# Optimization experiments

Measured on AMD Instinct MI355X. Metric: run time of the kernel, lower is better.

The kernel has to match this reference:

```python
import jax, jax.numpy as jnp
import numpy as np

A = 3                      # anchors per location
HS = [256, 128, 64, 32]    # square feature-map sizes (FPN levels)
B = 4                      # batch (num images)
SIZES = [A * h * h for h in HS]
T = sum(SIZES)             # 261120 anchors per image
PRE_N, POST_N = 512, 512
NMS_TH, SCORE_TH, MIN_SIZE = 0.7, 0.0, 1e-3
LOG_MAX = 4.135166556742356   # log(1000/16), standard delta clamp
MAXV = 8                      # max vertices of quad-quad intersection
LVL_OFF = 8192.0              # per-level coordinate offset for batched NMS


def box_corners(b):
    # b: [..., 5] (cx, cy, w, h, angle) -> [..., 4, 2] CCW corners
    cx, cy, w, h, a = (b[..., i] for i in range(5))
    c, s = jnp.cos(a), jnp.sin(a)
    dx = 0.5 * jnp.stack([w, -w, -w, w], -1)
    dy = 0.5 * jnp.stack([h, h, -h, -h], -1)
    x = cx[..., None] + dx * c[..., None] - dy * s[..., None]
    y = cy[..., None] + dx * s[..., None] + dy * c[..., None]
    return jnp.stack([x, y], -1)


def _clip(poly, cnt, p1, p2):
    # Sutherland-Hodgman clip of poly (padded [MAXV,2], cnt valid) by half-plane left of p1->p2
    e = p2 - p1
    d = e[0] * (poly[:, 1] - p1[1]) - e[1] * (poly[:, 0] - p1[0])
    def body(carry, i):
        out, oc = carry
        nxt = jnp.where(i + 1 < cnt, i + 1, 0)
        cur_in, nxt_in = d[i] >= 0, d[nxt] >= 0
        valid = i < cnt
        keep = valid & cur_in
        out = out.at[oc].set(jnp.where(keep, poly[i], out[oc]))
        oc = oc + keep.astype(jnp.int32)
        crs = valid & (cur_in != nxt_in)
        den = d[i] - d[nxt]
        t = d[i] / jnp.where(den == 0, 1.0, den)
        ip = poly[i] + t * (poly[nxt] - poly[i])
        out = out.at[oc].set(jnp.where(crs, ip, out[oc]))
        oc = oc + crs.astype(jnp.int32)
        return (out, oc), None
    (out, oc), _ = jax.lax.scan(body, (jnp.zeros((MAXV, 2), poly.dtype), jnp.int32(0)), jnp.arange(MAXV))
    return out, oc


def _inter_area(ca, cb):
    # intersection area of two convex quads given CCW corners [4,2]
    poly = jnp.zeros((MAXV, 2), ca.dtype).at[:4].set(ca)
    cnt = jnp.int32(4)
    for k in range(4):
        poly, cnt = _clip(poly, cnt, cb[k], cb[(k + 1) % 4])
    i = jnp.arange(MAXV)
    nxt = jnp.where(i + 1 < cnt, i + 1, 0)
    cr = poly[i, 0] * poly[nxt, 1] - poly[nxt, 0] * poly[i, 1]
    area = 0.5 * jnp.abs(jnp.sum(jnp.where(i < cnt, cr, 0.0)))
    return jnp.where(cnt >= 3, area, 0.0)


def decode(deltas, anchors):
    # XYWHA decode with 6-dim deltas (dx,dy,dw,dh,dsin,dcos), weights all 1.0
    ax, ay, aw, ah, aa = (anchors[..., i] for i in range(5))
    dx, dy, dw, dh, ds, dc = (deltas[..., i] for i in range(6))
    dw = jnp.minimum(dw, LOG_MAX)
    dh = jnp.minimum(dh, LOG_MAX)
    return jnp.stack([ax + dx * aw, ay + dy * ah, aw * jnp.exp(dw),
                      ah * jnp.exp(dh), aa + jnp.arctan2(ds, dc)], -1)


def nms_image(boxes, scores, levels):
    # boxes [N,5], scores [N] (post-sigmoid), levels [N] int32 -> fixed-size padded outputs
    N = scores.shape[0]
    valid = (boxes[:, 2] >= MIN_SIZE) & (boxes[:, 3] >= MIN_SIZE) & (scores >= SCORE_TH)
    s = jnp.where(valid, scores, -jnp.inf)
    order = jnp.argsort(-s)
    bx, sc, vd = boxes[order], s[order], valid[order]
    off = levels[order].astype(bx.dtype) * LVL_OFF
    nb = bx.at[:, :2].add(off[:, None])          # level offset => cross-level IoU == 0
    nbg = jax.lax.stop_gradient(nb)
    corners = box_corners(nbg)                    # [N,4,2]
    areas = nbg[:, 2] * nbg[:, 3]
    CH = 128
    def chunk_fn(args):
        cc, ca = args
        def row(ci, ai):
            inter = jax.vmap(lambda cj: _inter_area(ci, cj))(corners)
            return inter / (ai + areas - inter + 1e-7)
        return jax.vmap(row)(cc, ca)
    iou = jax.lax.map(chunk_fn, (corners.reshape(N // CH, CH, 4, 2),
                                 areas.reshape(N // CH, CH))).reshape(N, N)
    idx = jnp.arange(N)
    def body(i, sup):
        keep_i = ~sup[i]
        return sup | (keep_i & (iou[i] > NMS_TH) & (idx > i))
    sup = jax.lax.fori_loop(0, N, body, ~vd)      # invalid boxes start suppressed
    kept = ~sup
    _, top_i = jax.lax.top_k(jnp.where(kept, sc, -jnp.inf), POST_N)
    ok = kept[top_i]
    return jnp.where(ok[:, None], bx[top_i], 0.0), jnp.where(ok, sc[top_i], 0.0)


def rpn_forward(objs, dlts, anchors):
    obj_f, dlt_f = [], []
    for o, d, h in zip(objs, dlts, HS):
        # permute_and_flatten: [B,A,H,W] -> [B,H*W*A]; [B,A*6,H,W] -> [B,H*W*A,6]
        obj_f.append(o.transpose(0, 2, 3, 1).reshape(B, -1))
        dlt_f.append(d.reshape(B, A, 6, h, h).transpose(0, 3, 4, 1, 2).reshape(B, -1, 6))
    objectness = jnp.concatenate(obj_f, 1)        # [B, T]
    deltas = jnp.concatenate(dlt_f, 1)            # [B, T, 6]
    proposals = decode(deltas, anchors)           # [B, T, 5]
    parts, offset = [], 0
    for sz in SIZES:                               # per-level top-k
        k = min(PRE_N, sz)
        _, ti = jax.lax.top_k(objectness[:, offset:offset + sz], k)
        parts.append(ti + offset)
        offset += sz
    top_idx = jnp.concatenate(parts, 1)           # [B, 4*PRE_N]
    levels = jnp.concatenate([jnp.full((sz,), i, jnp.int32) for i, sz in enumerate(SIZES)])
    obj_top = jnp.take_along_axis(objectness, top_idx, 1)
    prop_top = jnp.take_along_axis(proposals, top_idx[..., None], 1)
    lvl_top = levels[top_idx]
    scores = jax.nn.sigmoid(obj_top)
    return jax.vmap(nms_image)(prop_top, scores, lvl_top)


def setup_inputs() -> dict:
    key = jax.random.key(0)
    ks = jax.random.split(key, 9)
    inp = {}
    for i, h in enumerate(HS):
        inp[f"obj{i}"] = jax.random.normal(ks[i], (B, A, h, h), jnp.float32)
        inp[f"dlt{i}"] = 0.25 * jax.random.normal(ks[4 + i], (B, A * 6, h, h), jnp.float32)
    u = jax.random.uniform(ks[8], (B, T, 5), jnp.float32)
    inp["anchors"] = jnp.stack([u[..., 0] * 1024.0, u[..., 1] * 1024.0,
                                8.0 + 120.0 * u[..., 2], 8.0 + 120.0 * u[..., 3],
                                jnp.pi * (u[..., 4] - 0.5)], -1)
    return inp


def reference(obj0, obj1, obj2, obj3, dlt0, dlt1, dlt2, dlt3, anchors):
    # returns (boxes [B, POST_N, 5], scores [B, POST_N]) padded with zeros
    return rpn_forward([obj0, obj1, obj2, obj3], [dlt0, dlt1, dlt2, dlt3], anchors)
```

## Files before the change

### kernel.cpp

```cpp
#include <hip/hip_runtime.h>

typedef unsigned int u32;
typedef unsigned long long u64;
typedef unsigned char u8;

#define NB 4
#define T_ANCH 261120
#define NCAND 2048
#define KSEL 512
#define POSTN 512
#define LOG_MAXF 4.135166556742356f
#define NMS_TH 0.7f
#define LVL_OFF_F 8192.0f
#define BINS 4096
#define EQCAP 8192
#define K5_BLOCKS 2048
#define K1_BLOCKS 256

__device__ __forceinline__ u32 mono32(float f){
  u32 u = __float_as_uint(f);
  return (u & 0x80000000u) ? ~u : (u | 0x80000000u);
}
__device__ __forceinline__ int lvl_hw(int lvl){ return 65536 >> (2*lvl); }
__device__ __forceinline__ int lvl_off(int lvl){
  return (lvl>0?196608:0) + (lvl>1?49152:0) + (lvl>2?12288:0);
}
__device__ __forceinline__ void k1_map(int bx, int& b, int& lvl, int& ch){
  b = bx >> 6;
  int c = bx & 63;
  if (c < 48){ lvl = 0; ch = c; }
  else if (c < 60){ lvl = 1; ch = c - 48; }
  else if (c < 63){ lvl = 2; ch = c - 60; }
  else { lvl = 3; ch = 0; }
}

__global__ __launch_bounds__(1024) void k1_hist_thresh(
    const float* __restrict__ o0, const float* __restrict__ o1,
    const float* __restrict__ o2, const float* __restrict__ o3,
    u32* __restrict__ hist16, u32* __restrict__ done16,
    u32* __restrict__ gb0, u32* __restrict__ gcA)
{
  int b, lvl, ch;
  k1_map(blockIdx.x, b, lvl, ch);
  int bid16 = b*4 + lvl;
  int nch = (lvl==0?48 : lvl==1?12 : lvl==2?3 : 1);
  const float* ob = (lvl==0)?o0 : (lvl==1)?o1 : (lvl==2)?o2 : o3;
  int hw = lvl_hw(lvl);
  int size = 3*hw;
  int n4 = size >> 2;
  int i4 = ch*1024 + threadIdx.x;
  __shared__ u32 hist[BINS];
  __shared__ u32 coarse[64];
  __shared__ int s_last;
  for (int i = threadIdx.x; i < BINS; i += 1024) hist[i] = 0;
  __syncthreads();
  if (i4 < n4){
    float4 v = ((const float4*)(ob + (size_t)b*size))[i4];
    atomicAdd(&hist[mono32(v.x) >> 20], 1u);
    atomicAdd(&hist[mono32(v.y) >> 20], 1u);
    atomicAdd(&hist[mono32(v.z) >> 20], 1u);
    atomicAdd(&hist[mono32(v.w) >> 20], 1u);
  }
  __syncthreads();
  u32* gh = hist16 + (size_t)bid16*BINS;
  for (int i = threadIdx.x; i < BINS; i += 1024){
    u32 c = hist[i];
    if (c) atomicAdd(&gh[i], c);
  }
  __syncthreads();
  if (threadIdx.x == 0){
    __threadfence();
    u32 d = atomicAdd(&done16[bid16], 1u);
    s_last = (d == (u32)(nch - 1)) ? 1 : 0;
  }
  __syncthreads();
  if (!s_last) return;

  __threadfence();
  for (int i = threadIdx.x; i < BINS; i += 1024)
    hist[i] = __hip_atomic_load(&gh[i], __ATOMIC_RELAXED, __HIP_MEMORY_SCOPE_AGENT);
  __syncthreads();
  int t = threadIdx.x;
  if (t < 64){
    u32 s = 0;
    for (int z = 0; z < 64; ++z) s += hist[t*64 + z];
    coarse[t] = s;
  }
  __syncthreads();
  if (t == 0){
    u32 acc = 0;
    int cb = 63;
    while (acc + coarse[cb] < (u32)KSEL){ acc += coarse[cb]; --cb; }
    int z = cb*64 + 63;
    while (acc + hist[z] < (u32)KSEL){ acc += hist[z]; --z; }
    gb0[bid16] = (u32)z;
    gcA[bid16] = acc;
  }
}

__global__ __launch_bounds__(1024) void k2_classify(
    const float* __restrict__ o0, const float* __restrict__ o1,
    const float* __restrict__ o2, const float* __restrict__ o3,
    const u32* __restrict__ gb0,
    u32* __restrict__ emitcnt, u32* __restrict__ tiecnt,
    int* __restrict__ cand_j, u64* __restrict__ gtie)
{
  int b, lvl, ch;
  k1_map(blockIdx.x, b, lvl, ch);
  int bid16 = b*4 + lvl;
  const float* ob = (lvl==0)?o0 : (lvl==1)?o1 : (lvl==2)?o2 : o3;
  int hw = lvl_hw(lvl);
  int size = 3*hw;
  int n4 = size >> 2;
  int i4 = ch*1024 + threadIdx.x;

  __shared__ u32 dbuf[KSEL];
  __shared__ u64 tbuf[4096];
  __shared__ u32 dn, tn, dbase, tbase;
  if (threadIdx.x == 0){ dn = 0; tn = 0; }
  __syncthreads();

  u32 b0v = gb0[bid16];
  if (i4 < n4){
    float4 v = ((const float4*)(ob + (size_t)b*size))[i4];
    int L = i4 << 2;
    int a = L / hw;
    int pix = L - a*hw;
    int j0 = pix*3 + a;
    float vv[4] = {v.x, v.y, v.z, v.w};
    #pragma unroll
    for (int q = 0; q < 4; ++q){
      u32 m = mono32(vv[q]);
      u32 bin = m >> 20;
      int j = j0 + 3*q;
      if (bin > b0v){
        u32 s = atomicAdd(&dn, 1u);
        if (s < (u32)KSEL) dbuf[s] = (u32)j;
      } else if (bin == b0v){
        u32 s = atomicAdd(&tn, 1u);
        if (s < 4096u) tbuf[s] = ((u64)m << 32) | (u32)(~(u32)j);
      }
    }
  }
  __syncthreads();
  if (threadIdx.x == 0){
    dbase = dn ? atomicAdd(&emitcnt[bid16], dn) : 0u;
    tbase = tn ? atomicAdd(&tiecnt[bid16], tn) : 0u;
  }
  __syncthreads();
  for (u32 x = threadIdx.x; x < dn; x += 1024){
    u32 s = dbase + x;
    if (s < (u32)KSEL) cand_j[bid16*KSEL + s] = (int)dbuf[x];
  }
  for (u32 x = threadIdx.x; x < tn; x += 1024){
    u32 s = tbase + x;
    if (s < (u32)EQCAP) gtie[(size_t)bid16*EQCAP + s] = tbuf[x];
  }
}

__global__ __launch_bounds__(512) void k3_tie_decode(
    const u64* __restrict__ gtie, const u32* __restrict__ tiecnt,
    const u32* __restrict__ gcA, const int* __restrict__ cand_j,
    const float* __restrict__ o0, const float* __restrict__ o1,
    const float* __restrict__ o2, const float* __restrict__ o3,
    const float* __restrict__ d0, const float* __restrict__ d1,
    const float* __restrict__ d2, const float* __restrict__ d3,
    const float* __restrict__ anchors,
    float* __restrict__ cscore, u32* __restrict__ csmono,
    u64* __restrict__ ctb, float* __restrict__ cbox, u8* __restrict__ cvalid)
{
  int bid = blockIdx.x;
  int t = threadIdx.x;
  __shared__ u64 eq[EQCAP];
  __shared__ u32 wbuf[KSEL];
  __shared__ int jlist[KSEL];
  __shared__ u32 wn;
  u32 n = tiecnt[bid]; if (n > (u32)EQCAP) n = (u32)EQCAP;
  u32 cA = gcA[bid];
  u32 k = (u32)KSEL - cA;
  if (t == 0) wn = 0;
  for (int i = t; i < KSEL; i += 512) jlist[i] = 0;
  for (u32 i = t; i < n; i += 512) eq[i] = gtie[(size_t)bid*EQCAP + i];
  __syncthreads();
  for (u32 i = t; i < n; i += 512){
    u64 ki = eq[i];
    u32 r = 0;
    for (u32 m = 0; m < n; ++m) r += (eq[m] > ki) ? 1u : 0u;
    if (r < k){
      u32 s = atomicAdd(&wn, 1u);
      if (s < (u32)KSEL) wbuf[s] = (u32)(~(u32)ki);
    }
  }
  __syncthreads();
  u32 w = wn;
  for (u32 i = t; i < cA; i += 512)
    if (i < (u32)KSEL) jlist[i] = cand_j[bid*KSEL + i];
  for (u32 x = t; x < w; x += 512){
    u32 s = cA + x;
    if (s < (u32)KSEL) jlist[s] = (int)wbuf[x];
  }
  __syncthreads();

  {
    int c = bid*KSEL + t;
    int b = bid >> 2, lvl = bid & 3;
    int j = jlist[t];
    int hw = lvl_hw(lvl);
    u32 pix = (u32)j / 3u;
    u32 a = (u32)j - pix*3u;
    const float* ob = (lvl==0)?o0 : (lvl==1)?o1 : (lvl==2)?o2 : o3;
    const float* dl = (lvl==0)?d0 : (lvl==1)?d1 : (lvl==2)?d2 : d3;

    float ov = ob[(size_t)(b*3 + (int)a)*hw + pix];
    size_t dbase = ((size_t)(b*3 + (int)a)*6)*(size_t)hw + pix;
    float dx  = dl[dbase + 0*(size_t)hw];
    float dy  = dl[dbase + 1*(size_t)hw];
    float dw  = dl[dbase + 2*(size_t)hw];
    float dh  = dl[dbase + 3*(size_t)hw];
    float dsn = dl[dbase + 4*(size_t)hw];
    float dcs = dl[dbase + 5*(size_t)hw];
    int tt = lvl_off(lvl) + j;
    const float* an = anchors + ((size_t)b*T_ANCH + tt)*5;
    float ax=an[0], ay=an[1], aw=an[2], ah=an[3], aa=an[4];
    dw = fminf(dw, LOG_MAXF); dh = fminf(dh, LOG_MAXF);
    float cx = ax + dx*aw;
    float cy = ay + dy*ah;
    float ww = aw * expf(dw);
    float hh = ah * expf(dh);
    float ang = aa + atan2f(dsn, dcs);
    double sd = 1.0 / (1.0 + exp(-(double)ov));
    float sc = (float)sd;
    bool valid = (ww >= 1e-3f) && (hh >= 1e-3f) && (sc >= 0.0f);
    cscore[c] = sc;
    csmono[c] = valid ? mono32(sc) : 0u;
    ctb[c] = ((u64)lvl << 50) | ((u64)(u32)(~mono32(ov)) << 18) | (u64)(u32)j;
    cvalid[c] = valid ? 1 : 0;
    float* bb = cbox + (size_t)c*5;
    bb[0]=cx; bb[1]=cy; bb[2]=ww; bb[3]=hh; bb[4]=ang;
  }
}

__global__ __launch_bounds__(256) void k4_rank(
    const u32* __restrict__ csmono, const u64* __restrict__ ctb,
    const float* __restrict__ cscore, const float* __restrict__ cbox,
    const u8* __restrict__ cvalid,
    float* __restrict__ sscore, float* __restrict__ sbox,
    float* __restrict__ geom, float4* __restrict__ aabb4,
    u8* __restrict__ svalid, u64* __restrict__ maskz, u64* __restrict__ rowflagz)
{
  int b   = blockIdx.x >> 6;
  int blk = blockIdx.x & 63;
  __shared__ u32 sm[NCAND];
  __shared__ u64 stb[NCAND];
  __shared__ u32 cnt[32][8];
  {
    u64* mz = maskz + (size_t)blockIdx.x * 1024;
    for (int x = threadIdx.x; x < 1024; x += 256) mz[x] = 0ull;
    if (threadIdx.x == 0 && blockIdx.x < NB*32) rowflagz[blockIdx.x] = 0ull;
  }
  for (int k = threadIdx.x; k < NCAND; k += 256){
    sm[k]  = csmono[b*NCAND + k];
    stb[k] = ctb[b*NCAND + k];
  }
  __syncthreads();
  int esub = threadIdx.x >> 3;
  int ssub = threadIdx.x & 7;
  int id = blk*32 + esub;
  u32 ms = sm[id];
  u64 mt = stb[id];
  u32 r = 0;
  #pragma unroll 8
  for (int it = 0; it < 256; ++it){
    int m = it*8 + ssub;
    u32 s2 = sm[m]; u64 t2 = stb[m];
    r += ((s2 > ms) || (s2 == ms && t2 < mt)) ? 1u : 0u;
  }
  cnt[esub][ssub] = r;
  __syncthreads();
  if (ssub == 0){
    u32 rank = 0;
    #pragma unroll
    for (int q = 0; q < 8; ++q) rank += cnt[esub][q];
    int gsrc = b*NCAND + id;
    int gdst = b*NCAND + (int)rank;
    sscore[gdst] = cscore[gsrc];
    svalid[gdst] = cvalid[gsrc];
    float b0 = cbox[(size_t)gsrc*5+0], b1 = cbox[(size_t)gsrc*5+1];
    float b2 = cbox[(size_t)gsrc*5+2], b3 = cbox[(size_t)gsrc*5+3];
    float b4 = cbox[(size_t)gsrc*5+4];
    float* sb = sbox + (size_t)gdst*5;
    sb[0]=b0; sb[1]=b1; sb[2]=b2; sb[3]=b3; sb[4]=b4;
    int lvl = (int)((mt >> 50) & 3ull);
    float offv = (float)lvl * LVL_OFF_F;
    float cx = b0 + offv, cy = b1 + offv, w=b2, h=b3, ang=b4;
    float cc = cosf(ang), sn = sinf(ang);
    float hx = 0.5f*w, hy = 0.5f*h;
    float x0 = cx + hx*cc - hy*sn, y0 = cy + hx*sn + hy*cc;
    float x1 = cx - hx*cc - hy*sn, y1 = cy - hx*sn + hy*cc;
    float x2 = cx - hx*cc + hy*sn, y2 = cy - hx*sn - hy*cc;
    float x3 = cx + hx*cc + hy*sn, y3 = cy + hx*sn - hy*cc;
    float minx = fminf(fminf(x0,x1),fminf(x2,x3));
    float maxx = fmaxf(fmaxf(x0,x1),fmaxf(x2,x3));
    float miny = fminf(fminf(y0,y1),fminf(y2,y3));
    float maxy = fmaxf(fmaxf(y0,y1),fmaxf(y2,y3));
    float* g = geom + (size_t)gdst*16;
    g[0]=minx; g[1]=maxx; g[2]=miny; g[3]=maxy; g[4]=w*h;
    g[5]=x0; g[6]=y0; g[7]=x1; g[8]=y1; g[9]=x2; g[10]=y2; g[11]=x3; g[12]=y3;
    aabb4[gdst] = make_float4(minx, maxx, miny, maxy);
  }
}

__device__ __forceinline__ void emit_pt(float* ox, float* oy, int oc, float x, float y){
  #pragma unroll
  for (int s = 0; s < 8; ++s) if (s == oc){ ox[s] = x; oy[s] = y; }
}

__device__ float quad_inter(const float* ca, const float* cb){
  float px[8], py[8];
  #pragma unroll
  for (int q = 0; q < 8; ++q){ px[q]=0.f; py[q]=0.f; }
  #pragma unroll
  for (int q = 0; q < 4; ++q){ px[q]=ca[2*q]; py[q]=ca[2*q+1]; }
  int cnt = 4;
  #pragma unroll
  for (int e = 0; e < 4; ++e){
    float p1x = cb[2*e],         p1y = cb[2*e+1];
    float p2x = cb[(2*e+2)&7],   p2y = cb[(2*e+3)&7];
    float ex = p2x-p1x, ey = p2y-p1y;
    float d[8];
    #pragma unroll
    for (int q = 0; q < 8; ++q) d[q] = ex*(py[q]-p1y) - ey*(px[q]-p1x);
    float ox[8], oy[8];
    #pragma unroll
    for (int q = 0; q < 8; ++q){ ox[q]=0.f; oy[q]=0.f; }
    int oc = 0;
    #pragma unroll
    for (int q = 0; q < 8; ++q){
      if (q < cnt){
        bool last = (q+1 >= cnt);
        float dn  = last ? d[0]  : d[(q+1)&7];
        bool in0 = (d[q] >= 0.0f), in1 = (dn >= 0.0f);
        if (in0){ emit_pt(ox,oy,oc,px[q],py[q]); oc++; }
        if (in0 != in1){
          float pnx = last ? px[0] : px[(q+1)&7];
          float pny = last ? py[0] : py[(q+1)&7];
          float den = d[q] - dn;
          float t = d[q] / ((den == 0.0f) ? 1.0f : den);
          emit_pt(ox,oy,oc, px[q] + t*(pnx-px[q]), py[q] + t*(pny-py[q]));
          oc++;
        }
      }
    }
    cnt = (oc > 8) ? 8 : oc;
    #pragma unroll
    for (int q = 0; q < 8; ++q){ px[q]=ox[q]; py[q]=oy[q]; }
  }
  if (cnt < 3) return 0.0f;
  float s = 0.0f;
  #pragma unroll
  for (int q = 0; q < 8; ++q){
    if (q < cnt){
      bool last = (q+1 >= cnt);
      float pnx = last ? px[0] : px[(q+1)&7];
      float pny = last ? py[0] : py[(q+1)&7];
      s += px[q]*pny - pnx*py[q];
    }
  }
  return 0.5f*fabsf(s);
}

__global__ __launch_bounds__(256) void k5_pairs(
    const float4* __restrict__ aabb4, const float* __restrict__ geom,
    u64* __restrict__ mask, u64* __restrict__ rowflag)
{
  __shared__ u32 lbuf[4096];
  __shared__ u32 lcnt;
  if (threadIdx.x == 0) lcnt = 0;
  __syncthreads();
  int img = blockIdx.x >> 9;
  int kk  = blockIdx.x & 511;
  int lane = threadIdx.x & 63;
  int rows[4] = {2*kk, 2*kk + 1, 2046 - 2*kk, 2047 - 2*kk};
  #pragma unroll
  for (int r = 0; r < 4; ++r){
    int i = rows[r];
    float4 gi = aabb4[img*NCAND + i];
    for (int j = i + 1 + (int)threadIdx.x; j < NCAND; j += 256){
      float4 gj = aabb4[img*NCAND + j];
      bool pass = !(gi.x > gj.y || gj.x > gi.y || gi.z > gj.w || gj.z > gi.w);
      u64 bm = __ballot(pass);
      if (bm){
        int leader = __ffsll((long long)bm) - 1;
        u32 base = 0;
        if (lane == leader) base = atomicAdd(&lcnt, (u32)__popcll(bm));
        base = (u32)__shfl((int)base, leader);
        if (pass){
          u32 off = (u32)__popcll(bm & ((1ull << lane) - 1ull));
          lbuf[base + off] = (u32)((i << 11) | j);
        }
      }
    }
  }
  __syncthreads();
  u32 n = lcnt;
  for (u32 x = threadIdx.x; x < n; x += 256){
    u32 gt = lbuf[x];
    int i = (int)(gt >> 11);
    int j = (int)(gt & (NCAND-1));
    const float* gi = geom + ((size_t)(img*NCAND + i))*16;
    const float* gj = geom + ((size_t)(img*NCAND + j))*16;
    float inter = quad_inter(gi+5, gj+5);
    float iou = inter / (gi[4] + gj[4] - inter + 1e-7f);
    if (iou > NMS_TH){
      atomicOr(&mask[((size_t)(img*NCAND + i))*32 + (j >> 6)], 1ull << (j & 63));
      atomicOr(&rowflag[(size_t)img*32 + (i >> 6)], 1ull << (i & 63));
    }
  }
}

__global__ __launch_bounds__(1024) void k6_nms_out(
    const u64* __restrict__ mask, const u64* __restrict__ rowflag,
    const u8* __restrict__ svalid,
    const float* __restrict__ sbox, const float* __restrict__ sscore,
    float* __restrict__ out)
{
  int b = blockIdx.x;
  __shared__ u32 fid[NCAND];
  __shared__ u32 wcnt[32], wpref[32];
  __shared__ u64 s_kept[32];
  __shared__ u32 pref[32];
  __shared__ u32 s_F;
  int t = threadIdx.x;
  int wid = t >> 6, lane = t & 63;

  if (t < 32) wcnt[t] = (u32)__popcll(rowflag[b*32 + t]);
  __syncthreads();
  if (t == 0){
    u32 run = 0;
    for (int w = 0; w < 32; ++w){ wpref[w] = run; run += wcnt[w]; }
    s_F = run;
  }
  __syncthreads();
  if (t < 32){
    u64 fw = rowflag[b*32 + t];
    u32 o = wpref[t];
    while (fw){
      int bpos = __builtin_ctzll(fw);
      fid[o++] = (u32)(t*64 + bpos);
      fw &= fw - 1;
    }
  }
  for (int x = t; x < POSTN*5; x += 1024) out[(size_t)b*POSTN*5 + x] = 0.0f;
  for (int x = t; x < POSTN;   x += 1024) out[(size_t)NB*POSTN*5 + b*POSTN + x] = 0.0f;
  __syncthreads();

  if (wid == 0){
    u32 slo = 0, shi = 0;
    {
      int wl = lane & 31;
      u64 w = 0;
      for (int q = 0; q < 64; ++q)
        if (!svalid[b*NCAND + wl*64 + q]) w |= (1ull << q);
      slo = (u32)w; shi = (u32)(w >> 32);
    }
    u32 F = s_F;
    const u64* mb = mask + ((size_t)b*NCAND)*32;
    for (u32 f = 0; f < F; f += 8){
      u32 myfid = 0;
      if (f + (lane & 7) < F) myfid = fid[f + (lane & 7)];
      u64 v[8];
      #pragma unroll
      for (int q = 0; q < 8; ++q){
        if (f + q < F){
          u32 fq = (u32)__builtin_amdgcn_readlane((int)myfid, q);
          v[q] = mb[(size_t)fq*32 + (lane & 31)];
        } else v[q] = 0ull;
      }
      #pragma unroll
      for (int q = 0; q < 8; ++q){
        if (f + q < F){
          u32 i = (u32)__builtin_amdgcn_readlane((int)myfid, q);
          int wi = (int)(i >> 6);
          u32 wlo = (u32)__builtin_amdgcn_readlane((int)slo, wi);
          u32 whi = (u32)__builtin_amdgcn_readlane((int)shi, wi);
          u64 w = ((u64)whi << 32) | wlo;
          u32 keep = (u32)((~w >> (i & 63)) & 1ull);
          u64 vm = v[q] & (0ull - (u64)keep);
          slo |= (u32)vm; shi |= (u32)(vm >> 32);
        }
      }
    }
    if (lane < 32) s_kept[lane] = ~(((u64)shi << 32) | slo);
  }
  __syncthreads();

  if (t < 32) pref[t] = (u32)__popcll(s_kept[t]);
  __syncthreads();
  if (t == 0){
    u32 run = 0;
    for (int w = 0; w < 32; ++w){ u32 tv = pref[w]; pref[w] = run; run += tv; }
  }
  __syncthreads();
  for (int i = t; i < NCAND; i += 1024){
    u64 kw = s_kept[i >> 6];
    if ((kw >> (i & 63)) & 1ull){
      u32 rank = pref[i >> 6] + (u32)__popcll(kw & ((1ull << (i & 63)) - 1ull));
      if (rank < POSTN){
        const float* bp = sbox + ((size_t)(b*NCAND + i))*5;
        float* op = out + ((size_t)(b*POSTN + rank))*5;
        op[0]=bp[0]; op[1]=bp[1]; op[2]=bp[2]; op[3]=bp[3]; op[4]=bp[4];
        out[(size_t)NB*POSTN*5 + b*POSTN + rank] = sscore[b*NCAND + i];
      }
    }
  }
}

extern "C" void kernel_launch(void* const* d_in, const int* in_sizes, int n_in,
                              void* d_out, int out_size, void* d_ws, size_t ws_size,
                              hipStream_t stream)
{
  (void)out_size; (void)ws_size;
  const float *obj[4] = {nullptr,nullptr,nullptr,nullptr};
  const float *dlt[4] = {nullptr,nullptr,nullptr,nullptr};
  const float *anchors = nullptr;
  for (int i = 0; i < n_in; ++i){
    int s = in_sizes[i];
    const float* p = (const float*)d_in[i];
    switch (s){
      case 786432:  obj[0] = p; break;
      case 4718592: dlt[0] = p; break;
      case 196608:  obj[1] = p; break;
      case 1179648: dlt[1] = p; break;
      case 49152:   obj[2] = p; break;
      case 294912:  dlt[2] = p; break;
      case 12288:   obj[3] = p; break;
      case 73728:   dlt[3] = p; break;
      case 5222400: anchors = p; break;
      default: break;
    }
  }

  char* wsb = (char*)d_ws;
  size_t off = 0;
  auto alloc = [&](size_t bytes)->void*{
    size_t cur = (off + 255) & ~(size_t)255;
    off = cur + bytes;
    return (void*)(wsb + cur);
  };
  int*   cand_j = (int*)  alloc(16*KSEL*sizeof(int));
  float* cscore = (float*)alloc((size_t)NB*NCAND*sizeof(float));
  u32*   csmono = (u32*)  alloc((size_t)NB*NCAND*sizeof(u32));
  u64*   ctb    = (u64*)  alloc((size_t)NB*NCAND*sizeof(u64));
  float* cbox   = (float*)alloc((size_t)NB*NCAND*5*sizeof(float));
  u8*    cvalid = (u8*)   alloc((size_t)NB*NCAND);
  float* sscore = (float*)alloc((size_t)NB*NCAND*sizeof(float));
  float* sbox   = (float*)alloc((size_t)NB*NCAND*5*sizeof(float));
  u8*    svalid = (u8*)   alloc((size_t)NB*NCAND);
  float* geom   = (float*)alloc((size_t)NB*NCAND*16*sizeof(float));
  float4* aabb4 = (float4*)alloc((size_t)NB*NCAND*sizeof(float4));
  u64*   gtie   = (u64*)  alloc((size_t)16*EQCAP*sizeof(u64));
  u64*   maskp  = (u64*)  alloc((size_t)NB*NCAND*32*sizeof(u64));
  u64*   rowflag= (u64*)  alloc((size_t)NB*32*sizeof(u64));
  u32*   gb0    = (u32*)  alloc(16*sizeof(u32));
  u32*   gcA    = (u32*)  alloc(16*sizeof(u32));
  u32*   hist16 = (u32*)  alloc((size_t)16*BINS*sizeof(u32));
  u32*   done16 = (u32*)  alloc(16*sizeof(u32));
  u32*   emitc  = (u32*)  alloc(16*sizeof(u32));
  u32*   tiec   = (u32*)  alloc(16*sizeof(u32));
  size_t zero_len = (size_t)((wsb + off) - (char*)hist16);

  hipMemsetAsync(hist16, 0, zero_len, stream);

  hipLaunchKernelGGL(k1_hist_thresh, dim3(K1_BLOCKS), dim3(1024), 0, stream,
                     obj[0], obj[1], obj[2], obj[3], hist16, done16, gb0, gcA);
  hipLaunchKernelGGL(k2_classify, dim3(K1_BLOCKS), dim3(1024), 0, stream,
                     obj[0], obj[1], obj[2], obj[3], gb0, emitc, tiec,
                     cand_j, gtie);
  hipLaunchKernelGGL(k3_tie_decode, dim3(16), dim3(512), 0, stream,
                     gtie, tiec, gcA, cand_j,
                     obj[0], obj[1], obj[2], obj[3],
                     dlt[0], dlt[1], dlt[2], dlt[3],
                     anchors, cscore, csmono, ctb, cbox, cvalid);
  hipLaunchKernelGGL(k4_rank, dim3(256), dim3(256), 0, stream,
                     csmono, ctb, cscore, cbox, cvalid, sscore, sbox, geom,
                     aabb4, svalid, maskp, rowflag);
  hipLaunchKernelGGL(k5_pairs, dim3(K5_BLOCKS), dim3(256), 0, stream,
                     aabb4, geom, maskp, rowflag);
  hipLaunchKernelGGL(k6_nms_out, dim3(4), dim3(1024), 0, stream,
                     maskp, rowflag, svalid, sbox, sscore, (float*)d_out);
}
```

Measured before the change: 192.3 us.

## Replace quadratic tie ranking with histogram radix select; widen NMS mask prefetch

The tie-decode kernel used to rank each tied candidate by comparing it against every other one, which is O(n^2) over up to 8192 entries. It now builds a 4096-bin histogram on key bits 40-51 and locates the threshold bin. Candidates above that bin are accepted directly, and only the threshold bin runs the quadratic ranking. Separately, the serial NMS mask-reduction loop now prefetches 16 mask rows per step instead of 8, hiding more load latency at the cost of more registers.

```diff
diff --git a/kernel.cpp b/kernel.cpp
--- a/kernel.cpp
+++ b/kernel.cpp
@@ -172,27 +172,63 @@
   int bid = blockIdx.x;
   int t = threadIdx.x;
   __shared__ u64 eq[EQCAP];
+  __shared__ u32 sidx[EQCAP];
+  __shared__ u32 hist2[4096];
+  __shared__ u32 coarse2[64];
   __shared__ u32 wbuf[KSEL];
   __shared__ int jlist[KSEL];
-  __shared__ u32 wn;
+  __shared__ u32 wn, sn, s_z2, s_acc2;
   u32 n = tiecnt[bid]; if (n > (u32)EQCAP) n = (u32)EQCAP;
   u32 cA = gcA[bid];
   u32 k = (u32)KSEL - cA;
-  if (t == 0) wn = 0;
+  if (t == 0){ wn = 0; sn = 0; }
   for (int i = t; i < KSEL; i += 512) jlist[i] = 0;
+  for (int i = t; i < 4096; i += 512) hist2[i] = 0;
   for (u32 i = t; i < n; i += 512) eq[i] = gtie[(size_t)bid*EQCAP + i];
   __syncthreads();
+  for (u32 i = t; i < n; i += 512)
+    atomicAdd(&hist2[(u32)(eq[i] >> 40) & 0xFFFu], 1u);
+  __syncthreads();
+  if (t < 64){
+    u32 s = 0;
+    for (int z = 0; z < 64; ++z) s += hist2[t*64 + z];
+    coarse2[t] = s;
+  }
+  __syncthreads();
+  if (t == 0){
+    u32 acc = 0;
+    int cb = 63;
+    while (cb > 0 && acc + coarse2[cb] < k){ acc += coarse2[cb]; --cb; }
+    int z = cb*64 + 63;
+    while (z > 0 && acc + hist2[z] < k){ acc += hist2[z]; --z; }
+    s_z2 = (u32)z; s_acc2 = acc;
+  }
+  __syncthreads();
+  u32 z2 = s_z2, acc2 = s_acc2;
   for (u32 i = t; i < n; i += 512){
-    u64 ki = eq[i];
+    u32 b2 = (u32)(eq[i] >> 40) & 0xFFFu;
+    if (b2 > z2){
+      u32 s = atomicAdd(&wn, 1u);
+      if (s < (u32)KSEL) wbuf[s] = (u32)(~(u32)eq[i]);
+    } else if (b2 == z2){
+      u32 s = atomicAdd(&sn, 1u);
+      if (s < (u32)EQCAP) sidx[s] = i;
+    }
+  }
+  __syncthreads();
+  u32 kk = k - acc2;
+  u32 ns = sn; if (ns > (u32)EQCAP) ns = (u32)EQCAP;
+  for (u32 x = t; x < ns; x += 512){
+    u64 ki = eq[sidx[x]];
     u32 r = 0;
-    for (u32 m = 0; m < n; ++m) r += (eq[m] > ki) ? 1u : 0u;
-    if (r < k){
+    for (u32 m2 = 0; m2 < ns; ++m2) r += (eq[sidx[m2]] > ki) ? 1u : 0u;
+    if (r < kk){
       u32 s = atomicAdd(&wn, 1u);
       if (s < (u32)KSEL) wbuf[s] = (u32)(~(u32)ki);
     }
   }
   __syncthreads();
-  u32 w = wn;
+  u32 w = wn; if (w > (u32)KSEL) w = (u32)KSEL;
   for (u32 i = t; i < cA; i += 512)
     if (i < (u32)KSEL) jlist[i] = cand_j[bid*KSEL + i];
   for (u32 x = t; x < w; x += 512){
@@ -465,19 +501,19 @@
     }
     u32 F = s_F;
     const u64* mb = mask + ((size_t)b*NCAND)*32;
-    for (u32 f = 0; f < F; f += 8){
+    for (u32 f = 0; f < F; f += 16){
       u32 myfid = 0;
-      if (f + (lane & 7) < F) myfid = fid[f + (lane & 7)];
-      u64 v[8];
+      if (f + (lane & 15) < F) myfid = fid[f + (lane & 15)];
+      u64 v[16];
       #pragma unroll
-      for (int q = 0; q < 8; ++q){
+      for (int q = 0; q < 16; ++q){
         if (f + q < F){
           u32 fq = (u32)__builtin_amdgcn_readlane((int)myfid, q);
           v[q] = mb[(size_t)fq*32 + (lane & 31)];
         } else v[q] = 0ull;
       }
       #pragma unroll
-      for (int q = 0; q < 8; ++q){
+      for (int q = 0; q < 16; ++q){
         if (f + q < F){
           u32 i = (u32)__builtin_amdgcn_readlane((int)myfid, q);
           int wi = (int)(i >> 6);
```

New measurement: 196.8 us. 2.3% more time.
